# Kernel tuning notes

Hardware: AMD Instinct MI355X
Metric: run time of the kernel (lower is better)

Reference implementation:

```python
import jax, jax.numpy as jnp
import numpy as np

MARGIN = 1.0


def setup_inputs() -> dict:
    key = jax.random.key(0)
    k1, k2, k3 = jax.random.split(key, 3)
    N, F = 4096, 512
    a = jax.random.normal(k1, (N, F), dtype=jnp.float32)
    b = jax.random.normal(k2, (N, F), dtype=jnp.float32)
    labels = jax.random.randint(k3, (N,), 0, 16, dtype=jnp.int32)
    return {"a": a, "b": b, "labels": labels}


def reference(a, b, labels):
    # D[i, j] = ||b_i - a_j||  (torch: Xa=a[None], Xb=b[:,None], sum over feat)
    # GEMM form of the pairwise sqdist; clamp tiny fp negatives before sqrt.
    Dsq = (jnp.sum(b * b, axis=1)[:, None]
           + jnp.sum(a * a, axis=1)[None, :]
           - 2.0 * (b @ a.T))
    D = jnp.sqrt(jnp.maximum(Dsq, 0.0))            # [N, N]
    Dexpm = jnp.exp(MARGIN - D)                    # [N, N]

    same = labels[:, None] == labels[None, :]      # [N, N]
    eye = jnp.eye(labels.shape[0], dtype=bool)
    pos_mask = same & ~eye                         # ordered positive pairs (i, j)
    neg_mask = ~same                               # negative pairs (labels differ)

    # neg_i sum for row i: sum_k Dexpm[i, k] over k with labels[k] != labels[i]
    row_negsum = jnp.sum(jnp.where(neg_mask, Dexpm, 0.0), axis=1)  # [N]

    # J_ij = log(neg_ik_sum + neg_jl_sum) + D[i, j]; hinged and squared
    J = jnp.log(row_negsum[:, None] + row_negsum[None, :]) + D
    hinge_sq = jnp.square(jnp.maximum(J, 0.0))

    num_pos = jnp.sum(pos_mask)
    return jnp.sum(jnp.where(pos_mask, hinge_sq, 0.0)) / (2.0 * num_pos)
```

## Files before the change

kernel.cpp:

```cpp
#include <hip/hip_runtime.h>
#include <math.h>

#define NROW 4096
#define FDIM 512
#define MARGIN 1.0f
#define NLAB 16
#define PREP_BLK 1024

typedef __attribute__((ext_vector_type(8))) short short8;
typedef __attribute__((ext_vector_type(4))) float floatx4;

__device__ inline unsigned short f2bf(float x) {
    unsigned u = __float_as_uint(x);
    return (unsigned short)((u + 0x7FFFu + ((u >> 16) & 1u)) >> 16);
}
__device__ inline void glds16(const unsigned short* g, unsigned short* l) {
    __builtin_amdgcn_global_load_lds(
        (const __attribute__((address_space(1))) unsigned int*)g,
        (__attribute__((address_space(3))) unsigned int*)l, 16, 0, 0);
}

__global__ __launch_bounds__(256) void prep_kernel(
    const float* __restrict__ a, const float* __restrict__ b,
    const int* __restrict__ labels,
    unsigned short* __restrict__ abf, unsigned short* __restrict__ bbf,
    float* __restrict__ na, float* __restrict__ nb,
    float* __restrict__ rns, float* __restrict__ loss,
    int* __restrict__ perm, int* __restrict__ goff,
    int* __restrict__ wl, int* __restrict__ wlmeta) {
    const int t = threadIdx.x;

    if (blockIdx.x == PREP_BLK) {
        __shared__ int hist[NLAB], off[NLAB], cur[NLAB];
        if (t < NLAB) hist[t] = 0;
        __syncthreads();
        for (int i = t; i < NROW; i += 256) atomicAdd(&hist[labels[i] & 15], 1);
        __syncthreads();
        if (t == 0) {
            int acc = 0;
            for (int g = 0; g < NLAB; ++g) { off[g] = acc; acc += hist[g]; }
            int n = 0;
            long long np = 0;
            for (int g = 0; g < NLAB; ++g) {
                goff[g] = off[g];
                int c = hist[g];
                np += (long long)c * (long long)(c - 1);
                int nt = (c + 63) >> 6;
                for (int ti = 0; ti < nt; ++ti)
                    for (int tj = 0; tj < nt; ++tj)
                        wl[n++] = (g << 12) | (ti << 6) | tj;
            }
            goff[NLAB] = NROW;
            wlmeta[0] = n;
            wlmeta[1] = (int)np;
            wlmeta[2] = 0;
            loss[0]   = 0.f;
        }
        __syncthreads();
        if (t < NLAB) cur[t] = off[t];
        __syncthreads();
        for (int i = t; i < NROW; i += 256) {
            int pos = atomicAdd(&cur[labels[i] & 15], 1);
            perm[pos] = i;
        }
        return;
    }

    const int grp = t >> 6;
    const int ln  = t & 63;
    const int row = blockIdx.x * 4 + grp;
    const float4* a4 = (const float4*)(a + (size_t)row * FDIM);
    const float4* b4 = (const float4*)(b + (size_t)row * FDIM);
    const int f = ln * 2;
    float4 va0 = a4[f], va1 = a4[f + 1];
    float4 vb0 = b4[f], vb1 = b4[f + 1];
    float sa = va0.x * va0.x + va0.y * va0.y + va0.z * va0.z + va0.w * va0.w
             + va1.x * va1.x + va1.y * va1.y + va1.z * va1.z + va1.w * va1.w;
    float sb = vb0.x * vb0.x + vb0.y * vb0.y + vb0.z * vb0.z + vb0.w * vb0.w
             + vb1.x * vb1.x + vb1.y * vb1.y + vb1.z * vb1.z + vb1.w * vb1.w;
    short8 ua, ub;
    ua[0] = (short)f2bf(va0.x); ua[1] = (short)f2bf(va0.y);
    ua[2] = (short)f2bf(va0.z); ua[3] = (short)f2bf(va0.w);
    ua[4] = (short)f2bf(va1.x); ua[5] = (short)f2bf(va1.y);
    ua[6] = (short)f2bf(va1.z); ua[7] = (short)f2bf(va1.w);
    ub[0] = (short)f2bf(vb0.x); ub[1] = (short)f2bf(vb0.y);
    ub[2] = (short)f2bf(vb0.z); ub[3] = (short)f2bf(vb0.w);
    ub[4] = (short)f2bf(vb1.x); ub[5] = (short)f2bf(vb1.y);
    ub[6] = (short)f2bf(vb1.z); ub[7] = (short)f2bf(vb1.w);
    *(short8*)&abf[(size_t)row * FDIM + (size_t)f * 4] = ua;
    *(short8*)&bbf[(size_t)row * FDIM + (size_t)f * 4] = ub;
    #pragma unroll
    for (int o = 32; o > 0; o >>= 1) {
        sa += __shfl_down(sa, o);
        sb += __shfl_down(sb, o);
    }
    if (ln == 0) {
        na[row] = sa;
        nb[row] = sb;
        rns[row] = 0.f;
    }
}

__global__ __launch_bounds__(512, 2) void pass_neg(
    const unsigned short* __restrict__ abf, const unsigned short* __restrict__ bbf,
    const int* __restrict__ labels,
    const float* __restrict__ na, const float* __restrict__ nb,
    float* __restrict__ rns)
{
    __shared__ __align__(16) unsigned short arena[65536];
    __shared__ float rpart[4][256];

    const int t    = threadIdx.x;
    const int lane = t & 63;
    const int w    = t >> 6;
    const int wi   = w >> 2;
    const int wj   = w & 3;
    const int lr   = lane & 15;
    const int lq   = lane >> 4;

    const int bid = blockIdx.x;
    const int wg  = (bid & 7) * 32 + (bid >> 3);
    const int by  = wg >> 4, bx = wg & 15;
    const int ti  = by * 256;
    const int tj  = bx * 256;

    floatx4 acc[8][4];
    #pragma unroll
    for (int i = 0; i < 8; ++i)
        #pragma unroll
        for (int j = 0; j < 4; ++j)
            acc[i][j] = (floatx4){0.f, 0.f, 0.f, 0.f};

    auto stage = [&](int kk, int buf) {
        unsigned short* As = arena + buf * 32768;
        unsigned short* Bs = As + 16384;
        #pragma unroll
        for (int l = 0; l < 4; ++l) {
            int c   = t + l * 512;
            int row = c >> 3;
            int qs  = (c & 7) ^ (row & 7);
            glds16(abf + (size_t)(tj + row) * FDIM + kk + qs * 8, As + c * 8);
            glds16(bbf + (size_t)(ti + row) * FDIM + kk + qs * 8, Bs + c * 8);
        }
    };

    stage(0, 0);
    __syncthreads();

    for (int it = 0; it < FDIM / 64; ++it) {
        if (it < FDIM / 64 - 1) stage((it + 1) * 64, (it + 1) & 1);

        const unsigned short* As = arena + (it & 1) * 32768;
        const unsigned short* Bs = As + 16384;
        #pragma unroll
        for (int s = 0; s < 2; ++s) {
            short8 af[8], bv[4];
            #pragma unroll
            for (int ri = 0; ri < 8; ++ri) {
                int R = wi * 128 + ri * 16 + lr;
                af[ri] = *(const short8*)
                    &Bs[R * 64 + (((s * 4 + lq) ^ (R & 7))) * 8];
            }
            #pragma unroll
            for (int rj = 0; rj < 4; ++rj) {
                int R = wj * 64 + rj * 16 + lr;
                bv[rj] = *(const short8*)
                    &As[R * 64 + (((s * 4 + lq) ^ (R & 7))) * 8];
            }
            #pragma unroll
            for (int ri = 0; ri < 8; ++ri)
                #pragma unroll
                for (int rj = 0; rj < 4; ++rj)
                    acc[ri][rj] = __builtin_amdgcn_mfma_f32_16x16x32_bf16(
                        af[ri], bv[rj], acc[ri][rj], 0, 0, 0);
        }
        __syncthreads();
    }

    int   ljv[4]; float najv[4];
    #pragma unroll
    for (int rj = 0; rj < 4; ++rj) {
        int jl = wj * 64 + rj * 16 + lr;
        ljv[rj]  = labels[tj + jl];
        najv[rj] = na[tj + jl];
    }
    #pragma unroll
    for (int ri = 0; ri < 8; ++ri) {
        float rs[4] = {0.f, 0.f, 0.f, 0.f};
        int liv[4]; float nbv[4];
        #pragma unroll
        for (int r = 0; r < 4; ++r) {
            int il = wi * 128 + ri * 16 + lq * 4 + r;
            liv[r] = labels[ti + il];
            nbv[r] = nb[ti + il];
        }
        #pragma unroll
        for (int rj = 0; rj < 4; ++rj)
            #pragma unroll
            for (int r = 0; r < 4; ++r) {
                if (liv[r] != ljv[rj]) {
                    float dsq = nbv[r] + najv[rj] - 2.f * acc[ri][rj][r];
                    float D   = sqrtf(fmaxf(dsq, 0.f));
                    rs[r] += __expf(MARGIN - D);
                }
            }
        #pragma unroll
        for (int r = 0; r < 4; ++r) {
            #pragma unroll
            for (int o = 8; o > 0; o >>= 1) rs[r] += __shfl_down(rs[r], o, 16);
        }
        if (lr == 0) {
            #pragma unroll
            for (int r = 0; r < 4; ++r)
                rpart[wj][wi * 128 + ri * 16 + lq * 4 + r] = rs[r];
        }
    }
    __syncthreads();
    if (t < 256) {
        float s = rpart[0][t] + rpart[1][t] + rpart[2][t] + rpart[3][t];
        atomicAdd(&rns[ti + t], s);
    }
}

__global__ __launch_bounds__(256) void pass2_pos(
    const unsigned short* __restrict__ abf, const unsigned short* __restrict__ bbf,
    const float* __restrict__ na, const float* __restrict__ nb,
    const float* __restrict__ rns,
    const int* __restrict__ perm, const int* __restrict__ goff,
    const int* __restrict__ wl, const int* __restrict__ wlmeta,
    float* __restrict__ loss_sum, int* __restrict__ done,
    float* __restrict__ out)
{
    __shared__ __align__(16) unsigned short arena[16384];
    __shared__ int   rows_i[64], rows_j[64];
    __shared__ float rbi_s[64], rbj_s[64], nbi_s[64], naj_s[64];
    __shared__ float part[4];

    const int t    = threadIdx.x;
    const int lane = t & 63;
    const int w    = t >> 6;
    const int wi   = w >> 1, wj = w & 1;
    const int lr   = lane & 15;
    const int lq   = lane >> 4;
    const int nwl  = wlmeta[0];

    float local = 0.f;

    for (int item = blockIdx.x; item < nwl; item += gridDim.x) {
        __syncthreads();
        int e  = wl[item];
        int g  = e >> 12, ti = (e >> 6) & 63, tj = e & 63;
        int gb = goff[g], ge = goff[g + 1];
        int cnt = ge - gb;

        if (t < 64) {
            int idx = gb + ti * 64 + t;
            int ig  = perm[idx < ge ? idx : gb];
            rows_i[t] = ig;
            rbi_s[t]  = rns[ig];
            nbi_s[t]  = nb[ig];
        } else if (t < 128) {
            int u   = t - 64;
            int idx = gb + tj * 64 + u;
            int jg  = perm[idx < ge ? idx : gb];
            rows_j[u] = jg;
            rbj_s[u]  = rns[jg];
            naj_s[u]  = na[jg];
        }
        __syncthreads();

        floatx4 acc[2][2];
        #pragma unroll
        for (int i = 0; i < 2; ++i)
            #pragma unroll
            for (int j = 0; j < 2; ++j)
                acc[i][j] = (floatx4){0.f, 0.f, 0.f, 0.f};

        auto stage = [&](int kk) {
            #pragma unroll
            for (int l = 0; l < 4; ++l) {
                int c   = t + l * 256;
                int row = c >> 4;
                int qs  = (c & 15) ^ (row & 7);
                glds16(abf + (size_t)rows_j[row] * FDIM + kk + qs * 8,
                       arena + c * 8);
                glds16(bbf + (size_t)rows_i[row] * FDIM + kk + qs * 8,
                       arena + 8192 + c * 8);
            }
        };

        stage(0);
        __syncthreads();

        #pragma unroll
        for (int itk = 0; itk < 4; ++itk) {
            const unsigned short* As = arena;
            const unsigned short* Bs = arena + 8192;
            #pragma unroll
            for (int ks = 0; ks < 4; ++ks) {
                short8 af[2], bfv[2];
                #pragma unroll
                for (int ri = 0; ri < 2; ++ri) {
                    int R = wi * 32 + ri * 16 + lr;
                    af[ri] = *(const short8*)
                        &Bs[R * 128 + (((ks * 4 + lq) ^ (R & 7))) * 8];
                }
                #pragma unroll
                for (int rj = 0; rj < 2; ++rj) {
                    int R = wj * 32 + rj * 16 + lr;
                    bfv[rj] = *(const short8*)
                        &As[R * 128 + (((ks * 4 + lq) ^ (R & 7))) * 8];
                }
                #pragma unroll
                for (int ri = 0; ri < 2; ++ri)
                    #pragma unroll
                    for (int rj = 0; rj < 2; ++rj)
                        acc[ri][rj] = __builtin_amdgcn_mfma_f32_16x16x32_bf16(
                            af[ri], bfv[rj], acc[ri][rj], 0, 0, 0);
            }
            if (itk < 3) {
                __syncthreads();
                stage((itk + 1) * 128);
                __syncthreads();
            }
        }

        #pragma unroll
        for (int ri = 0; ri < 2; ++ri)
            #pragma unroll
            for (int rj = 0; rj < 2; ++rj) {
                int  jl  = wj * 32 + rj * 16 + lr;
                bool vj  = (tj * 64 + jl) < cnt;
                int  jg  = rows_j[jl];
                float nav = naj_s[jl], rbj = rbj_s[jl];
                #pragma unroll
                for (int r = 0; r < 4; ++r) {
                    int  il = wi * 32 + ri * 16 + lq * 4 + r;
                    bool vi = (ti * 64 + il) < cnt;
                    if (vi && vj && rows_i[il] != jg) {
                        float dsq = nbi_s[il] + nav - 2.f * acc[ri][rj][r];
                        float D   = sqrtf(fmaxf(dsq, 0.f));
                        float J   = __logf(rbi_s[il] + rbj) + D;
                        float h   = fmaxf(J, 0.f);
                        local += h * h;
                    }
                }
            }
    }

    #pragma unroll
    for (int o = 32; o > 0; o >>= 1) local += __shfl_down(local, o);
    if (lane == 0) part[w] = local;
    __syncthreads();
    if (t == 0) {
        atomicAdd(loss_sum, part[0] + part[1] + part[2] + part[3]);
        __threadfence();
        int old = atomicAdd(done, 1);
        if (old == (int)gridDim.x - 1) {
            __threadfence();
            float total = *(volatile float*)loss_sum;
            out[0] = total / (2.0f * (float)wlmeta[1]);
        }
    }
}

extern "C" void kernel_launch(void* const* d_in, const int* in_sizes, int n_in,
                              void* d_out, int out_size, void* d_ws, size_t ws_size,
                              hipStream_t stream) {
    const float* a      = (const float*)d_in[0];
    const float* b      = (const float*)d_in[1];
    const int*   labels = (const int*)d_in[2];
    float* out = (float*)d_out;

    unsigned short* abf = (unsigned short*)d_ws;
    unsigned short* bbf = abf + (size_t)NROW * FDIM;
    float* fws  = (float*)(bbf + (size_t)NROW * FDIM);
    float* na   = fws;
    float* nb   = fws + NROW;
    float* rns  = fws + 2 * NROW;
    float* loss = fws + 3 * NROW;
    int* iws    = (int*)(fws + 3 * NROW + 4);
    int* perm   = iws;
    int* goff   = iws + NROW;
    int* wlmeta = iws + NROW + 20;
    int* wl     = iws + NROW + 24;

    prep_kernel<<<PREP_BLK + 1, 256, 0, stream>>>(a, b, labels, abf, bbf,
                                                  na, nb, rns, loss,
                                                  perm, goff, wl, wlmeta);
    pass_neg<<<(NROW / 256) * (NROW / 256), 512, 0, stream>>>(abf, bbf, labels,
                                                              na, nb, rns);
    pass2_pos<<<256, 256, 0, stream>>>(abf, bbf, na, nb, rns, perm, goff, wl,
                                       wlmeta, loss, &wlmeta[2], out);
}
```

Measured before the change: 135.9 us.

## Triple-buffer pass_neg K-loop and double-buffer pass2_pos loads with vmcnt barriers

pass_neg now uses K-steps of 32 with a three-stage LDS ring and a new XOR swizzle. Two tiles are kept in flight, and an explicit s_waitcnt vmcnt plus s_barrier replaces __syncthreads, with setprio raised around the MFMA block. pass2_pos gains a second LDS buffer so the next K chunk loads while the current one computes, and its grid grows from 256 to 384 blocks. The aim is to hide global-to-LDS latency behind matrix math. In exchange there are more barriers per K, more LDS in pass2_pos, and fragile hand-counted vmcnt values.

```diff
diff --git a/kernel.cpp b/kernel.cpp
--- a/kernel.cpp
+++ b/kernel.cpp
@@ -19,6 +19,12 @@
         (const __attribute__((address_space(1))) unsigned int*)g,
         (__attribute__((address_space(3))) unsigned int*)l, 16, 0, 0);
 }
+#define WAIT_VM_BARRIER(N)                                          \
+    do {                                                            \
+        asm volatile("s_waitcnt vmcnt(" #N ")" ::: "memory");       \
+        __builtin_amdgcn_s_barrier();                               \
+        __builtin_amdgcn_sched_barrier(0);                          \
+    } while (0)
 
 __global__ __launch_bounds__(256) void prep_kernel(
     const float* __restrict__ a, const float* __restrict__ b,
@@ -107,7 +113,7 @@
     const float* __restrict__ na, const float* __restrict__ nb,
     float* __restrict__ rns)
 {
-    __shared__ __align__(16) unsigned short arena[65536];
+    __shared__ __align__(16) unsigned short arena[49152];
     __shared__ float rpart[4][256];
 
     const int t    = threadIdx.x;
@@ -132,49 +138,55 @@
             acc[i][j] = (floatx4){0.f, 0.f, 0.f, 0.f};
 
     auto stage = [&](int kk, int buf) {
-        unsigned short* As = arena + buf * 32768;
-        unsigned short* Bs = As + 16384;
-        #pragma unroll
-        for (int l = 0; l < 4; ++l) {
+        unsigned short* As = arena + buf * 16384;
+        unsigned short* Bs = As + 8192;
+        #pragma unroll
+        for (int l = 0; l < 2; ++l) {
             int c   = t + l * 512;
-            int row = c >> 3;
-            int qs  = (c & 7) ^ (row & 7);
+            int row = c >> 2;
+            int qs  = (c & 3) ^ ((row >> 1) & 3);
             glds16(abf + (size_t)(tj + row) * FDIM + kk + qs * 8, As + c * 8);
             glds16(bbf + (size_t)(ti + row) * FDIM + kk + qs * 8, Bs + c * 8);
         }
     };
 
     stage(0, 0);
-    __syncthreads();
-
-    for (int it = 0; it < FDIM / 64; ++it) {
-        if (it < FDIM / 64 - 1) stage((it + 1) * 64, (it + 1) & 1);
-
-        const unsigned short* As = arena + (it & 1) * 32768;
-        const unsigned short* Bs = As + 16384;
-        #pragma unroll
-        for (int s = 0; s < 2; ++s) {
-            short8 af[8], bv[4];
-            #pragma unroll
-            for (int ri = 0; ri < 8; ++ri) {
-                int R = wi * 128 + ri * 16 + lr;
-                af[ri] = *(const short8*)
-                    &Bs[R * 64 + (((s * 4 + lq) ^ (R & 7))) * 8];
-            }
-            #pragma unroll
-            for (int rj = 0; rj < 4; ++rj) {
-                int R = wj * 64 + rj * 16 + lr;
-                bv[rj] = *(const short8*)
-                    &As[R * 64 + (((s * 4 + lq) ^ (R & 7))) * 8];
-            }
-            #pragma unroll
-            for (int ri = 0; ri < 8; ++ri)
-                #pragma unroll
-                for (int rj = 0; rj < 4; ++rj)
-                    acc[ri][rj] = __builtin_amdgcn_mfma_f32_16x16x32_bf16(
-                        af[ri], bv[rj], acc[ri][rj], 0, 0, 0);
-        }
-        __syncthreads();
+    stage(32, 1);
+    WAIT_VM_BARRIER(4);
+
+    #pragma unroll
+    for (int it = 0; it < 16; ++it) {
+        if (it < 14) stage((it + 2) * 32, (it + 2) % 3);
+
+        const unsigned short* As = arena + (it % 3) * 16384;
+        const unsigned short* Bs = As + 8192;
+        short8 af[8], bv[4];
+        #pragma unroll
+        for (int ri = 0; ri < 8; ++ri) {
+            int R = wi * 128 + ri * 16 + lr;
+            af[ri] = *(const short8*)
+                &Bs[R * 32 + ((lq ^ ((R >> 1) & 3))) * 8];
+        }
+        #pragma unroll
+        for (int rj = 0; rj < 4; ++rj) {
+            int R = wj * 64 + rj * 16 + lr;
+            bv[rj] = *(const short8*)
+                &As[R * 32 + ((lq ^ ((R >> 1) & 3))) * 8];
+        }
+        __builtin_amdgcn_s_setprio(1);
+        #pragma unroll
+        for (int ri = 0; ri < 8; ++ri)
+            #pragma unroll
+            for (int rj = 0; rj < 4; ++rj)
+                acc[ri][rj] = __builtin_amdgcn_mfma_f32_16x16x32_bf16(
+                    af[ri], bv[rj], acc[ri][rj], 0, 0, 0);
+        __builtin_amdgcn_s_setprio(0);
+
+        if (it < 14) {
+            WAIT_VM_BARRIER(4);
+        } else if (it == 14) {
+            WAIT_VM_BARRIER(0);
+        }
     }
 
     int   ljv[4]; float najv[4];
@@ -231,7 +243,7 @@
     float* __restrict__ loss_sum, int* __restrict__ done,
     float* __restrict__ out)
 {
-    __shared__ __align__(16) unsigned short arena[16384];
+    __shared__ __align__(16) unsigned short arena[32768];
     __shared__ int   rows_i[64], rows_j[64];
     __shared__ float rbi_s[64], rbj_s[64], nbi_s[64], naj_s[64];
     __shared__ float part[4];
@@ -276,26 +288,30 @@
             for (int j = 0; j < 2; ++j)
                 acc[i][j] = (floatx4){0.f, 0.f, 0.f, 0.f};
 
-        auto stage = [&](int kk) {
+        auto stage = [&](int kk, int buf) {
+            unsigned short* As = arena + buf * 16384;
+            unsigned short* Bs = As + 8192;
             #pragma unroll
             for (int l = 0; l < 4; ++l) {
                 int c   = t + l * 256;
                 int row = c >> 4;
                 int qs  = (c & 15) ^ (row & 7);
                 glds16(abf + (size_t)rows_j[row] * FDIM + kk + qs * 8,
-                       arena + c * 8);
+                       As + c * 8);
                 glds16(bbf + (size_t)rows_i[row] * FDIM + kk + qs * 8,
-                       arena + 8192 + c * 8);
+                       Bs + c * 8);
             }
         };
 
-        stage(0);
-        __syncthreads();
+        stage(0, 0);
+        WAIT_VM_BARRIER(0);
 
         #pragma unroll
         for (int itk = 0; itk < 4; ++itk) {
-            const unsigned short* As = arena;
-            const unsigned short* Bs = arena + 8192;
+            if (itk < 3) stage((itk + 1) * 128, (itk + 1) & 1);
+
+            const unsigned short* As = arena + (itk & 1) * 16384;
+            const unsigned short* Bs = As + 8192;
             #pragma unroll
             for (int ks = 0; ks < 4; ++ks) {
                 short8 af[2], bfv[2];
@@ -318,11 +334,7 @@
                         acc[ri][rj] = __builtin_amdgcn_mfma_f32_16x16x32_bf16(
                             af[ri], bfv[rj], acc[ri][rj], 0, 0, 0);
             }
-            if (itk < 3) {
-                __syncthreads();
-                stage((itk + 1) * 128);
-                __syncthreads();
-            }
+            if (itk < 3) WAIT_VM_BARRIER(0);
         }
 
         #pragma unroll
@@ -390,6 +402,6 @@
                                                   perm, goff, wl, wlmeta);
     pass_neg<<<(NROW / 256) * (NROW / 256), 512, 0, stream>>>(abf, bbf, labels,
                                                               na, nb, rns);
-    pass2_pos<<<256, 256, 0, stream>>>(abf, bbf, na, nb, rns, perm, goff, wl,
+    pass2_pos<<<384, 256, 0, stream>>>(abf, bbf, na, nb, rns, perm, goff, wl,
                                        wlmeta, loss, &wlmeta[2], out);
 }
```

After: 130.7 us. -3.9%, faster.
